# Performance work log

Measured on AMD Instinct MI355X. Metric: run time of the kernel, lower is better.

## Reference

```python
import jax, jax.numpy as jnp
import numpy as np

N_NODES = 100000
N_EDGES = 1600000
D = 128
OUT = 2

def setup_inputs() -> dict:
    key = jax.random.key(0)
    k1, k2, k3, k4, k5 = jax.random.split(key, 5)
    h = jax.random.normal(k1, (N_NODES, D), dtype=jnp.float32)
    src = jax.random.randint(k2, (N_EDGES,), 0, N_NODES, dtype=jnp.int64)
    dst = jax.random.randint(k3, (N_EDGES,), 0, N_NODES, dtype=jnp.int64)
    # Linear(2*D, OUT): weight [OUT, 2*D], bias [OUT] (torch convention)
    bound = 1.0 / np.sqrt(2 * D)
    W = jax.random.uniform(k4, (OUT, 2 * D), dtype=jnp.float32, minval=-bound, maxval=bound)
    b = jax.random.uniform(k5, (OUT,), dtype=jnp.float32, minval=-bound, maxval=bound)
    return {"h": h, "src": src, "dst": dst, "W": W, "b": b}

def reference(h, src, dst, W, b):
    # Gather src/dst node features per edge, concat, apply linear.
    h_u = h[src]  # [E, D]
    h_v = h[dst]  # [E, D]
    # Avoid materializing concat by splitting W: W = [W_u | W_v]
    W_u, W_v = W[:, :D], W[:, D:]
    score = h_u @ W_u.T + h_v @ W_v.T + b  # [E, OUT]
    return score
```

## Files before the change

kernel.cpp:

```cpp
#include <hip/hip_runtime.h>


#define DIM 128

__global__ __launch_bounds__(256) void node_project(const float* __restrict__ h,
                                                    const float* __restrict__ W,
                                                    const float* __restrict__ b,
                                                    float4* __restrict__ pq,
                                                    int n_nodes) {
    int gtid = blockIdx.x * blockDim.x + threadIdx.x;
    int wave = gtid >> 6;
    int lane = threadIdx.x & 63;
    int half = lane >> 5;
    int j    = lane & 31;
    int node = wave * 2 + half;

    const float4* W4 = (const float4*)W;
    float4 wu0 = W4[j];
    float4 wv0 = W4[32 + j];
    float4 wu1 = W4[64 + j];
    float4 wv1 = W4[96 + j];

    float4 hv = make_float4(0.f, 0.f, 0.f, 0.f);
    if (node < n_nodes)
        hv = ((const float4*)(h + (size_t)node * DIM))[j];

    float su0 = hv.x*wu0.x + hv.y*wu0.y + hv.z*wu0.z + hv.w*wu0.w;
    float su1 = hv.x*wu1.x + hv.y*wu1.y + hv.z*wu1.z + hv.w*wu1.w;
    float sv0 = hv.x*wv0.x + hv.y*wv0.y + hv.z*wv0.z + hv.w*wv0.w;
    float sv1 = hv.x*wv1.x + hv.y*wv1.y + hv.z*wv1.z + hv.w*wv1.w;

    #pragma unroll
    for (int m = 16; m >= 1; m >>= 1) {
        su0 += __shfl_xor(su0, m);
        su1 += __shfl_xor(su1, m);
        sv0 += __shfl_xor(sv0, m);
        sv1 += __shfl_xor(sv1, m);
    }

    if (j == 0 && node < n_nodes) {
        pq[node] = make_float4(su0 + b[0], su1 + b[1], sv0, sv1);
    }
}

__global__ __launch_bounds__(256) void edge_gather(const int* __restrict__ src,
                                                   const int* __restrict__ dst,
                                                   const float4* __restrict__ pq,
                                                   float* __restrict__ out,
                                                   int n_edges) {
    int t = blockIdx.x * blockDim.x + threadIdx.x;
    int e0 = t * 2;
    if (e0 + 1 < n_edges) {
        int2 s = ((const int2*)src)[t];
        int2 d = ((const int2*)dst)[t];
        float4 a0 = pq[s.x];
        float4 c0 = pq[d.x];
        float4 a1 = pq[s.y];
        float4 c1 = pq[d.y];
        float4 o;
        o.x = a0.x + c0.z;
        o.y = a0.y + c0.w;
        o.z = a1.x + c1.z;
        o.w = a1.y + c1.w;
        ((float4*)out)[t] = o;
    } else if (e0 < n_edges) {
        int s = src[e0], d = dst[e0];
        float4 a = pq[s];
        float4 c = pq[d];
        out[(size_t)e0 * 2 + 0] = a.x + c.z;
        out[(size_t)e0 * 2 + 1] = a.y + c.w;
    }
}

extern "C" void kernel_launch(void* const* d_in, const int* in_sizes, int n_in,
                              void* d_out, int out_size, void* d_ws, size_t ws_size,
                              hipStream_t stream) {
    const float* h   = (const float*)d_in[0];
    const int*   src = (const int*)d_in[1];
    const int*   dst = (const int*)d_in[2];
    const float* W   = (const float*)d_in[3];
    const float* b   = (const float*)d_in[4];
    float*       out = (float*)d_out;

    int n_nodes = in_sizes[0] / DIM;
    int n_edges = in_sizes[1];

    float4* pq = (float4*)d_ws;

    int blocks1 = (n_nodes + 7) / 8;
    node_project<<<blocks1, 256, 0, stream>>>(h, W, b, pq, n_nodes);

    int n_threads = (n_edges + 1) / 2;
    int blocks2 = (n_threads + 255) / 256;
    edge_gather<<<blocks2, 256, 0, stream>>>(src, dst, pq, out, n_edges);
}
```

Before: 117.8 us.

## Fuse node projection and edge gather into one cooperative persistent kernel

Merges the two launches into a single cooperative kernel with a fixed grid of 1024 blocks. Blocks grid-stride over nodes to build the projected table, wait at a grid-wide barrier, then grid-stride over edge pairs for the gather. The aim is to drop the second launch and the gap between kernels. In exchange it adds the cost of a grid sync and caps the number of resident blocks, which can reduce latency hiding in the memory-bound gather.

```diff
diff --git a/kernel.cpp b/kernel.cpp
--- a/kernel.cpp
+++ b/kernel.cpp
@@ -1,74 +1,81 @@
 #include <hip/hip_runtime.h>
+#include <hip/hip_cooperative_groups.h>
+
+namespace cg = cooperative_groups;
 
 
 #define DIM 128
+#define GRID_BLOCKS 1024
+#define BLOCK_THREADS 256
 
-__global__ __launch_bounds__(256) void node_project(const float* __restrict__ h,
-                                                    const float* __restrict__ W,
-                                                    const float* __restrict__ b,
-                                                    float4* __restrict__ pq,
-                                                    int n_nodes) {
-    int gtid = blockIdx.x * blockDim.x + threadIdx.x;
-    int wave = gtid >> 6;
+__global__ __launch_bounds__(BLOCK_THREADS)
+void fused_edge_mlp(const float* __restrict__ h,
+                    const float* __restrict__ W,
+                    const float* __restrict__ b,
+                    const int* __restrict__ src,
+                    const int* __restrict__ dst,
+                    float4* __restrict__ pq,
+                    float* __restrict__ out,
+                    int n_nodes, int n_edges) {
     int lane = threadIdx.x & 63;
     int half = lane >> 5;
     int j    = lane & 31;
-    int node = wave * 2 + half;
+    int gwave = (blockIdx.x * BLOCK_THREADS + threadIdx.x) >> 6;
+    const int nodes_per_sweep = GRID_BLOCKS * (BLOCK_THREADS / 64) * 2;
 
     const float4* W4 = (const float4*)W;
     float4 wu0 = W4[j];
     float4 wv0 = W4[32 + j];
     float4 wu1 = W4[64 + j];
     float4 wv1 = W4[96 + j];
+    float b0 = b[0], b1 = b[1];
 
-    float4 hv = make_float4(0.f, 0.f, 0.f, 0.f);
-    if (node < n_nodes)
-        hv = ((const float4*)(h + (size_t)node * DIM))[j];
+    for (int node = gwave * 2 + half; node < n_nodes; node += nodes_per_sweep) {
+        float4 hv = ((const float4*)(h + (size_t)node * DIM))[j];
 
-    float su0 = hv.x*wu0.x + hv.y*wu0.y + hv.z*wu0.z + hv.w*wu0.w;
-    float su1 = hv.x*wu1.x + hv.y*wu1.y + hv.z*wu1.z + hv.w*wu1.w;
-    float sv0 = hv.x*wv0.x + hv.y*wv0.y + hv.z*wv0.z + hv.w*wv0.w;
-    float sv1 = hv.x*wv1.x + hv.y*wv1.y + hv.z*wv1.z + hv.w*wv1.w;
+        float su0 = hv.x*wu0.x + hv.y*wu0.y + hv.z*wu0.z + hv.w*wu0.w;
+        float su1 = hv.x*wu1.x + hv.y*wu1.y + hv.z*wu1.z + hv.w*wu1.w;
+        float sv0 = hv.x*wv0.x + hv.y*wv0.y + hv.z*wv0.z + hv.w*wv0.w;
+        float sv1 = hv.x*wv1.x + hv.y*wv1.y + hv.z*wv1.z + hv.w*wv1.w;
 
-    #pragma unroll
-    for (int m = 16; m >= 1; m >>= 1) {
-        su0 += __shfl_xor(su0, m);
-        su1 += __shfl_xor(su1, m);
-        sv0 += __shfl_xor(sv0, m);
-        sv1 += __shfl_xor(sv1, m);
+        #pragma unroll
+        for (int m = 16; m >= 1; m >>= 1) {
+            su0 += __shfl_xor(su0, m);
+            su1 += __shfl_xor(su1, m);
+            sv0 += __shfl_xor(sv0, m);
+            sv1 += __shfl_xor(sv1, m);
+        }
+
+        if (j == 0)
+            pq[node] = make_float4(su0 + b0, su1 + b1, sv0, sv1);
     }
 
-    if (j == 0 && node < n_nodes) {
-        pq[node] = make_float4(su0 + b[0], su1 + b[1], sv0, sv1);
-    }
-}
+    cg::this_grid().sync();
 
-__global__ __launch_bounds__(256) void edge_gather(const int* __restrict__ src,
-                                                   const int* __restrict__ dst,
-                                                   const float4* __restrict__ pq,
-                                                   float* __restrict__ out,
-                                                   int n_edges) {
-    int t = blockIdx.x * blockDim.x + threadIdx.x;
-    int e0 = t * 2;
-    if (e0 + 1 < n_edges) {
-        int2 s = ((const int2*)src)[t];
-        int2 d = ((const int2*)dst)[t];
-        float4 a0 = pq[s.x];
-        float4 c0 = pq[d.x];
-        float4 a1 = pq[s.y];
-        float4 c1 = pq[d.y];
-        float4 o;
-        o.x = a0.x + c0.z;
-        o.y = a0.y + c0.w;
-        o.z = a1.x + c1.z;
-        o.w = a1.y + c1.w;
-        ((float4*)out)[t] = o;
-    } else if (e0 < n_edges) {
-        int s = src[e0], d = dst[e0];
-        float4 a = pq[s];
-        float4 c = pq[d];
-        out[(size_t)e0 * 2 + 0] = a.x + c.z;
-        out[(size_t)e0 * 2 + 1] = a.y + c.w;
+    int n_thr = (n_edges + 1) / 2;
+    const int stride = GRID_BLOCKS * BLOCK_THREADS;
+    for (int t = blockIdx.x * BLOCK_THREADS + threadIdx.x; t < n_thr; t += stride) {
+        int e0 = t * 2;
+        if (e0 + 1 < n_edges) {
+            int2 s = ((const int2*)src)[t];
+            int2 d = ((const int2*)dst)[t];
+            float4 a0 = pq[s.x];
+            float4 c0 = pq[d.x];
+            float4 a1 = pq[s.y];
+            float4 c1 = pq[d.y];
+            float4 o;
+            o.x = a0.x + c0.z;
+            o.y = a0.y + c0.w;
+            o.z = a1.x + c1.z;
+            o.w = a1.y + c1.w;
+            ((float4*)out)[t] = o;
+        } else {
+            int s = src[e0], d = dst[e0];
+            float4 a = pq[s];
+            float4 c = pq[d];
+            out[(size_t)e0 * 2 + 0] = a.x + c.z;
+            out[(size_t)e0 * 2 + 1] = a.y + c.w;
+        }
     }
 }
 
@@ -87,10 +94,9 @@
 
     float4* pq = (float4*)d_ws;
 
-    int blocks1 = (n_nodes + 7) / 8;
-    node_project<<<blocks1, 256, 0, stream>>>(h, W, b, pq, n_nodes);
-
-    int n_threads = (n_edges + 1) / 2;
-    int blocks2 = (n_threads + 255) / 256;
-    edge_gather<<<blocks2, 256, 0, stream>>>(src, dst, pq, out, n_edges);
+    void* args[] = {(void*)&h, (void*)&W, (void*)&b, (void*)&src, (void*)&dst,
+                    (void*)&pq, (void*)&out, (void*)&n_nodes, (void*)&n_edges};
+    hipLaunchCooperativeKernel((void*)fused_edge_mlp,
+                               dim3(GRID_BLOCKS), dim3(BLOCK_THREADS),
+                               args, 0, stream);
 }
```

New measurement: 234.9 us. 99.4% more time.
